# Performance work log

Measured on AMD Instinct MI355X. Metric: run time of the kernel, lower is better.

Reference implementation:

```python
import jax, jax.numpy as jnp
import numpy as np

D = 256      # feature_dim (d_model)
H = 4        # num_heads
N = 4096     # query nodes
M = 4096     # source nodes


def _conv1x1(W, b, x):
    # Conv1d(kernel_size=1): per-position linear over channels. x: [1, Cin, N]
    return jnp.einsum('oi,bin->bon', W, x) + b[None, :, None]


def setup_inputs() -> dict:
    key = jax.random.key(0)
    ks = jax.random.split(key, 16)
    s = 0.02
    inp = {
        'x':      jax.random.normal(ks[0], (1, D, N), jnp.float32),
        'source': jax.random.normal(ks[1], (1, D, M), jnp.float32),
        'dist':   jax.random.uniform(ks[2], (1, N, M), jnp.float32),
        'mask':   jax.random.bernoulli(ks[3], 0.5, (N, M)),
        'Wq': s * jax.random.normal(ks[4], (D, D), jnp.float32),  'bq': jnp.zeros((D,), jnp.float32),
        'Wk': s * jax.random.normal(ks[5], (D, D), jnp.float32),  'bk': jnp.zeros((D,), jnp.float32),
        'Wv': s * jax.random.normal(ks[6], (D, D), jnp.float32),  'bv': jnp.zeros((D,), jnp.float32),
        'Wm': s * jax.random.normal(ks[7], (D, D), jnp.float32),  'bm': jnp.zeros((D,), jnp.float32),
        'W1': s * jax.random.normal(ks[8], (2 * D, 2 * D), jnp.float32), 'b1': jnp.zeros((2 * D,), jnp.float32),
        'W2': s * jax.random.normal(ks[9], (D, 2 * D), jnp.float32),     'b2': jnp.zeros((D,), jnp.float32),
    }
    return inp


def reference(x, source, dist, mask, Wq, bq, Wk, bk, Wv, bv, Wm, bm, W1, b1, W2, b2):
    dim = D // H  # per-head dim; torch view(1, dim, H, -1) splits channels as (dim, H)
    q = _conv1x1(Wq, bq, x).reshape(1, dim, H, N)
    k = _conv1x1(Wk, bk, source).reshape(1, dim, H, M)
    v = _conv1x1(Wv, bv, source).reshape(1, dim, H, M)

    scores = jnp.einsum('bdhn,bdhm->bhnm', q, k) / jnp.sqrt(jnp.asarray(dim, q.dtype))
    # non-standard additive mask: global detached min scales the masked-out entries
    smin = jax.lax.stop_gradient(scores.min())
    scores = scores + smin * (~mask).astype(scores.dtype)[None, None, :, :]

    prob = jax.nn.softmax(scores, axis=-1)                       # [1,H,N,M]
    attn = jnp.einsum('bhnm,bdhm->bdhn', prob, v)                # [1,dim,H,N]
    message = _conv1x1(Wm, bm, attn.reshape(1, D, N))            # merge heads

    h = jnp.concatenate([x, message], axis=1)                    # [1,2D,N]
    h = jax.nn.relu(_conv1x1(W1, b1, h))
    y = _conv1x1(W2, b2, h)                                      # [1,D,N]
    weights = scores.mean(axis=1)                                # [1,N,M]
    return y, weights
```

## Files before the change

### kernel.cpp

```cpp
#include <hip/hip_runtime.h>
#include <hip/hip_bf16.h>
#include <hip/hip_fp16.h>
#include <math.h>

#define Dm 256
#define Hh 4
#define Nn 4096
#define Mq 4096

typedef __attribute__((ext_vector_type(8))) short bf16x8;
typedef __attribute__((ext_vector_type(4))) float f32x4;
typedef _Float16 __attribute__((ext_vector_type(4))) f16x4;
typedef __fp16 __attribute__((ext_vector_type(2))) h16x2;

#define MFMA_BF16(a,b,c) __builtin_amdgcn_mfma_f32_16x16x32_bf16(a,b,c,0,0,0)
#define MFMA_F16x16(a,b,c) __builtin_amdgcn_mfma_f32_16x16x16f16(a,b,c,0,0,0)

#define MB (1u<<20)
#define OFF_FLAG  0
#define OFF_SMIN  64
#define OFF_KMAX  128
#define OFF_MT    8192
#define OFF_DENP  (128u<<10)
#define OFF_WB    (3u*MB/2)
#define OFF_BITS  (3u*MB)
#define OFF_ATTNT (3u*MB)
#define OFF_QB    (5u*MB)
#define OFF_KB    (7u*MB)
#define OFF_VB    (9u*MB)
#define OFF_HCAT  (11u*MB)
#define OFF_OPART (15u*MB)
#define OFF_XT    (17u*MB)
#define OFF_ST    (19u*MB)
#define OFF_H1T   (15u*MB)

#define WOFF_Q  0
#define WOFF_K  65536
#define WOFF_V  131072
#define WOFF_M  196608
#define WOFF_1  262144
#define WOFF_2  524288

__device__ __forceinline__ unsigned short f2bf(float x) {
    unsigned u = __float_as_uint(x);
    u += 0x7FFF + ((u >> 16) & 1);
    return (unsigned short)(u >> 16);
}
__device__ __forceinline__ float bf2f(unsigned short b) {
    return __uint_as_float(((unsigned)b) << 16);
}
__device__ __forceinline__ unsigned fkey(float f) {
    unsigned u = __float_as_uint(f);
    return (u & 0x80000000u) ? ~u : (u | 0x80000000u);
}
__device__ __forceinline__ float fdecode(unsigned k) {
    return (k & 0x80000000u) ? __uint_as_float(k ^ 0x80000000u) : __uint_as_float(~k);
}

__global__ __launch_bounds__(256) void k_prep(const float* __restrict__ x,
                                              const float* __restrict__ source,
                                              unsigned short* __restrict__ xt,
                                              unsigned short* __restrict__ st,
                                              unsigned short* __restrict__ hcat,
                                              const unsigned char* __restrict__ maskb,
                                              int* __restrict__ flag,
                                              unsigned* __restrict__ kmax,
                                              unsigned* __restrict__ sminkey) {
    const int z = blockIdx.z;
    const float* src = z ? source : x;
    unsigned short* dst = z ? st : xt;
    unsigned short* dst2 = z ? nullptr : hcat;
    const int l = threadIdx.x & 63, g = threadIdx.x >> 6;
    const int c = blockIdx.y * 64 + l;
    const int n0 = blockIdx.x * 32 + g * 8;
    float4 v0 = *(const float4*)(src + (size_t)c * Nn + n0);
    float4 v1 = *(const float4*)(src + (size_t)c * Nn + n0 + 4);
    float vv[8] = {v0.x, v0.y, v0.z, v0.w, v1.x, v1.y, v1.z, v1.w};
    #pragma unroll
    for (int j = 0; j < 8; j++) {
        unsigned short b = f2bf(vv[j]);
        dst[(size_t)(n0 + j) * 256 + c] = b;
        if (dst2) dst2[(size_t)(n0 + j) * 512 + c] = b;
    }
    if (blockIdx.x == 0 && blockIdx.y == 0 && z == 0) {
        __shared__ int cnt[5];
        if (threadIdx.x < 5) cnt[threadIdx.x] = 0;
        if (threadIdx.x < 4) kmax[threadIdx.x] = 0u;
        if (threadIdx.x == 0) *sminkey = 0xFFFFFFFFu;
        __syncthreads();
        for (int i = threadIdx.x; i < 16384; i += 256) {
            unsigned char b = maskb[i];
            if (b) {
                atomicAdd(&cnt[i & 3], 1);
                if ((i & 7) == 4) atomicAdd(&cnt[4], 1);
            }
        }
        __syncthreads();
        if (threadIdx.x == 0) {
            int f;
            if (cnt[3] > 0 && cnt[0] == 0)        f = 3;
            else if (cnt[1] | cnt[2] | cnt[3])    f = 1;
            else if (cnt[4] > 0)                  f = 0;
            else                                  f = 2;
            *flag = f;
        }
    }
}

__global__ void k_maskbits(const void* __restrict__ mp, const int* __restrict__ flagp,
                           unsigned char* __restrict__ bits) {
    size_t i = (size_t)blockIdx.x * 256 + threadIdx.x;
    const int flag = *flagp;
    size_t base = i * 8;
    unsigned b = 0;
    if (flag == 1) {
        unsigned long long u = *(const unsigned long long*)((const unsigned char*)mp + base);
        #pragma unroll
        for (int j = 0; j < 8; j++) b |= (unsigned)(((u >> (8*j)) & 0xFFull) != 0ull) << j;
    } else if (flag == 0) {
        const int* p = (const int*)mp;
        #pragma unroll
        for (int j = 0; j < 8; j++) b |= (unsigned)(p[base + j] != 0) << j;
    } else if (flag == 3) {
        const float* p = (const float*)mp;
        #pragma unroll
        for (int j = 0; j < 8; j++) b |= (unsigned)(p[base + j] != 0.0f) << j;
    } else {
        const unsigned long long* p = (const unsigned long long*)mp;
        #pragma unroll
        for (int j = 0; j < 8; j++) b |= (unsigned)(p[base + j] != 0ull) << j;
    }
    bits[i] = (unsigned char)b;
}

__global__ void k_wcast(const float* __restrict__ Wq, const float* __restrict__ Wk,
                        const float* __restrict__ Wv, const float* __restrict__ Wm,
                        const float* __restrict__ W1, const float* __restrict__ W2,
                        unsigned short* __restrict__ wb) {
    size_t i = (size_t)blockIdx.x * 256 + threadIdx.x;
    const float* s; size_t off;
    if      (i < 65536)               { s = Wq; off = i; }
    else if (i < 131072)              { s = Wk; off = i - 65536; }
    else if (i < 196608)              { s = Wv; off = i - 131072; }
    else if (i < 262144)              { s = Wm; off = i - 196608; }
    else if (i < 524288)              { s = W1; off = i - 262144; }
    else                              { s = W2; off = i - 524288; }
    wb[i] = f2bf(s[off]);
}

template<int KK, int JT>
__device__ __forceinline__ void gemm_body(const unsigned short* __restrict__ wb,
                                          const float* __restrict__ bias,
                                          const unsigned short* __restrict__ xt,
                                          void* __restrict__ out, int mode,
                                          int bx, int by) {
    const int tid = threadIdx.x, w = tid >> 6, lane = tid & 63;
    const int lg = lane >> 4, lr = lane & 15;
    const int o_base = by * 64 + w * 16;
    const int n_base = bx * (16 * JT);
    f32x4 acc[JT];
    #pragma unroll
    for (int j = 0; j < JT; j++) acc[j] = (f32x4){0.f, 0.f, 0.f, 0.f};
    const unsigned short* wrow = wb + (size_t)(o_base + lr) * KK + lg * 8;
    const unsigned short* xrow = xt + (size_t)(n_base + lr) * KK + lg * 8;
    #pragma unroll
    for (int k0 = 0; k0 < KK; k0 += 32) {
        bf16x8 af = *(const bf16x8*)(wrow + k0);
        #pragma unroll
        for (int j = 0; j < JT; j++) {
            bf16x8 bfr = *(const bf16x8*)(xrow + (size_t)j * 16 * KK + k0);
            acc[j] = MFMA_BF16(af, bfr, acc[j]);
        }
    }
    float bv[4];
    #pragma unroll
    for (int r = 0; r < 4; r++) bv[r] = bias[o_base + lg * 4 + r];
    #pragma unroll
    for (int j = 0; j < JT; j++) {
        #pragma unroll
        for (int r = 0; r < 4; r++) {
            int o = o_base + lg * 4 + r;
            int n = n_base + j * 16 + lr;
            float v = acc[j][r] + bv[r];
            if (mode == 0) {
                ((float*)out)[(size_t)o * Nn + n] = v;
            } else if (mode == 1) {
                ((unsigned short*)out)[(((size_t)(o & 3)) * Nn + n) * 64 + (o >> 2)] = f2bf(v);
            } else if (mode == 2) {
                union { _Float16 h; unsigned short u; } cv; cv.h = (_Float16)v;
                ((unsigned short*)out)[(((size_t)(o & 3)) * 64 + (o >> 2)) * Mq + n] = cv.u;
            } else if (mode == 3) {
                ((unsigned short*)out)[(size_t)n * 512 + 256 + o] = f2bf(v);
            } else if (mode == 4) {
                ((unsigned short*)out)[(size_t)n * 512 + o] = f2bf(fmaxf(v, 0.f));
            } else {
                int dd = o >> 2, hh = o & 3, g = dd >> 3, pos = dd & 7;
                int slot = g ^ (n & 7);
                ((unsigned short*)out)[(((size_t)hh * Mq + n)) * 64 + slot * 8 + pos] = f2bf(v);
            }
        }
    }
}

template<int KK, int JT>
__global__ __launch_bounds__(256) void k_mgemm(const unsigned short* __restrict__ wb,
                                               const float* __restrict__ bias,
                                               const unsigned short* __restrict__ xt,
                                               void* __restrict__ out, int mode) {
    gemm_body<KK, JT>(wb, bias, xt, out, mode, blockIdx.x, blockIdx.y);
}

__global__ __launch_bounds__(256) void k_qkv(const unsigned short* __restrict__ wb,
                                             const float* __restrict__ bq,
                                             const float* __restrict__ bk,
                                             const float* __restrict__ bv,
                                             const unsigned short* __restrict__ xt,
                                             const unsigned short* __restrict__ st,
                                             void* __restrict__ qb, void* __restrict__ kb,
                                             void* __restrict__ vb) {
    const int z = blockIdx.z;
    const float* bias = (z == 0) ? bq : ((z == 1) ? bk : bv);
    const unsigned short* X = (z == 0) ? xt : st;
    void* out = (z == 0) ? qb : ((z == 1) ? kb : vb);
    int mode = (z == 0) ? 1 : ((z == 1) ? 5 : 2);
    gemm_body<256, 4>(wb + z * 65536, bias, X, out, mode, blockIdx.x, blockIdx.y);
}

__global__ __launch_bounds__(256) void k_knorm(const unsigned short* __restrict__ kb,
                                               unsigned* __restrict__ kmax) {
    const int h = blockIdx.y;
    const int m = blockIdx.x * 256 + threadIdx.x;
    const unsigned short* row = kb + ((size_t)(h * Mq + m) << 6);
    float s = 0.f;
    #pragma unroll
    for (int i = 0; i < 64; i++) { float v = bf2f(row[i]); s = fmaf(v, v, s); }
    __shared__ float red[256];
    red[threadIdx.x] = s;
    __syncthreads();
    for (int st = 128; st > 0; st >>= 1) {
        if (threadIdx.x < st) red[threadIdx.x] = fmaxf(red[threadIdx.x], red[threadIdx.x + st]);
        __syncthreads();
    }
    if (threadIdx.x == 0) atomicMax(kmax + h, __float_as_uint(red[0]));
}

__global__ __launch_bounds__(256) void k_qnorm(const unsigned short* __restrict__ qb,
                                               const unsigned* __restrict__ kmax,
                                               float* __restrict__ mtarr) {
    const int row = blockIdx.x * 256 + threadIdx.x;
    const unsigned short* qr = qb + ((size_t)row << 6);
    float s = 0.f;
    #pragma unroll
    for (int i = 0; i < 64; i++) { float v = bf2f(qr[i]); s = fmaf(v, v, s); }
    float k2 = __uint_as_float(kmax[row >> 12]);
    mtarr[row] = sqrtf(s * k2) * 0.125f;
}

__global__ __launch_bounds__(256) void k_min(
    const unsigned short* __restrict__ qb, const unsigned short* __restrict__ kb,
    unsigned* __restrict__ sminkey) {
    __shared__ unsigned short kbuf[2][8192];
    const int tid = threadIdx.x;
    const int w = tid >> 6, lane = tid & 63;
    const int lg = lane >> 4, lr = lane & 15;
    const int n0 = blockIdx.x * 128 + w * 32;
    const int m0 = blockIdx.y * 128;

    bf16x8 qf[4][2][2];
    #pragma unroll
    for (int h = 0; h < 4; h++)
        #pragma unroll
        for (int ns = 0; ns < 2; ns++)
            #pragma unroll
            for (int kh = 0; kh < 2; kh++)
                qf[h][ns][kh] = *(const bf16x8*)(qb + (((size_t)h * Nn + n0 + ns*16 + lr) << 6) + kh*32 + lg*8);

    const unsigned short* srcs[4];
    #pragma unroll
    for (int h = 0; h < 4; h++) srcs[h] = kb + (((size_t)h * Mq + m0) << 6) + tid * 8;

    float mn = INFINITY;

    bf16x8 r[4];
    #pragma unroll
    for (int h = 0; h < 4; h++) {
        r[h] = *(const bf16x8*)(srcs[h]);
        *(bf16x8*)&kbuf[0][h * 2048 + tid * 8] = r[h];
    }
    __syncthreads();
    #pragma unroll
    for (int h = 0; h < 4; h++) r[h] = *(const bf16x8*)(srcs[h] + 2048);

    for (int t = 0; t < 4; t++) {
        const unsigned short* kB = &kbuf[t & 1][0];
        #pragma unroll
        for (int mi = 0; mi < 2; mi++) {
            const int rowoff = (mi * 16 + lr) * 64;
            #pragma unroll
            for (int h = 0; h < 4; h++) {
                bf16x8 a0 = *(const bf16x8*)(kB + h*2048 + rowoff + ((lg ^ (lr & 7)) << 3));
                bf16x8 a1 = *(const bf16x8*)(kB + h*2048 + rowoff + (((lg + 4) ^ (lr & 7)) << 3));
                #pragma unroll
                for (int ns = 0; ns < 2; ns++) {
                    f32x4 acc = (f32x4){0.f, 0.f, 0.f, 0.f};
                    acc = MFMA_BF16(a0, qf[h][ns][0], acc);
                    acc = MFMA_BF16(a1, qf[h][ns][1], acc);
                    mn = fminf(mn, fminf(fminf(acc[0], acc[1]), fminf(acc[2], acc[3])));
                }
            }
        }
        if (t < 3) {
            #pragma unroll
            for (int h = 0; h < 4; h++)
                *(bf16x8*)&kbuf[(t + 1) & 1][h * 2048 + tid * 8] = r[h];
        }
        __syncthreads();
        if (t < 2) {
            #pragma unroll
            for (int h = 0; h < 4; h++) r[h] = *(const bf16x8*)(srcs[h] + (size_t)(t + 2) * 2048);
        }
    }

    for (int off = 1; off < 64; off <<= 1) mn = fminf(mn, __shfl_xor(mn, off));
    __shared__ float wmin[4];
    if (lane == 0) wmin[w] = mn;
    __syncthreads();
    if (tid == 0) {
        float m2 = fminf(fminf(wmin[0], wmin[1]), fminf(wmin[2], wmin[3]));
        atomicMin(sminkey, fkey(m2 * 0.125f));
    }
}

__global__ __launch_bounds__(256) void k_wout(
    const unsigned short* __restrict__ qb, const unsigned short* __restrict__ kb,
    const unsigned long long* __restrict__ bits,
    const unsigned* __restrict__ skey, float* __restrict__ wout) {
    __shared__ unsigned short kbuf[2][8192];
    const int tid = threadIdx.x;
    const int w = tid >> 6, lane = tid & 63;
    const int lg = lane >> 4, lr = lane & 15;
    const int n0 = blockIdx.x * 128 + w * 32;
    const int m0 = blockIdx.y * 128;
    const float smin = fdecode(*skey);

    bf16x8 qf[4][2][2];
    #pragma unroll
    for (int h = 0; h < 4; h++)
        #pragma unroll
        for (int ns = 0; ns < 2; ns++)
            #pragma unroll
            for (int kh = 0; kh < 2; kh++)
                qf[h][ns][kh] = *(const bf16x8*)(qb + (((size_t)h * Nn + n0 + ns*16 + lr) << 6) + kh*32 + lg*8);

    const unsigned short* srcs[4];
    #pragma unroll
    for (int h = 0; h < 4; h++) srcs[h] = kb + (((size_t)h * Mq + m0) << 6) + tid * 8;

    const unsigned long long* brow0 = bits + (((size_t)(n0 + lr)) << 6) + (m0 >> 6);
    const unsigned long long* brow1 = bits + (((size_t)(n0 + 16 + lr)) << 6) + (m0 >> 6);
    unsigned long long bw0 = 0ull, bw1 = 0ull;

    bf16x8 r[4];
    #pragma unroll
    for (int h = 0; h < 4; h++) {
        r[h] = *(const bf16x8*)(srcs[h]);
        *(bf16x8*)&kbuf[0][h * 2048 + tid * 8] = r[h];
    }
    __syncthreads();
    #pragma unroll
    for (int h = 0; h < 4; h++) r[h] = *(const bf16x8*)(srcs[h] + 2048);

    for (int t = 0; t < 4; t++) {
        const unsigned short* kB = &kbuf[t & 1][0];
        const int mch = m0 + t * 32;
        if ((t & 1) == 0) { bw0 = brow0[t >> 1]; bw1 = brow1[t >> 1]; }
        #pragma unroll
        for (int mi = 0; mi < 2; mi++) {
            const int rowoff = (mi * 16 + lr) * 64;
            f32x4 acc[2][2];
            #pragma unroll
            for (int ns = 0; ns < 2; ns++) {
                acc[ns][0] = (f32x4){0.f, 0.f, 0.f, 0.f};
                acc[ns][1] = (f32x4){0.f, 0.f, 0.f, 0.f};
            }
            #pragma unroll
            for (int h = 0; h < 4; h++) {
                bf16x8 a0 = *(const bf16x8*)(kB + h*2048 + rowoff + ((lg ^ (lr & 7)) << 3));
                bf16x8 a1 = *(const bf16x8*)(kB + h*2048 + rowoff + (((lg + 4) ^ (lr & 7)) << 3));
                const int hf = h >> 1;
                #pragma unroll
                for (int ns = 0; ns < 2; ns++) {
                    acc[ns][hf] = MFMA_BF16(a0, qf[h][ns][0], acc[ns][hf]);
                    acc[ns][hf] = MFMA_BF16(a1, qf[h][ns][1], acc[ns][hf]);
                }
            }
            const int shb = (t & 1) * 32 + mi * 16 + lg * 4;
            #pragma unroll
            for (int ns = 0; ns < 2; ns++) {
                unsigned long long bw = ns ? bw1 : bw0;
                f32x4 wv;
                #pragma unroll
                for (int rr = 0; rr < 4; rr++) {
                    bool b = (bw >> (shb + rr)) & 1ull;
                    wv[rr] = fmaf(acc[ns][0][rr] + acc[ns][1][rr], 0.03125f, b ? 0.f : smin);
                }
                __builtin_nontemporal_store(wv,
                    (f32x4*)(wout + (size_t)(n0 + ns*16 + lr) * Mq + mch + mi * 16 + lg * 4));
            }
        }
        if (t < 3) {
            #pragma unroll
            for (int h = 0; h < 4; h++)
                *(bf16x8*)&kbuf[(t + 1) & 1][h * 2048 + tid * 8] = r[h];
        }
        __syncthreads();
        if (t < 2) {
            #pragma unroll
            for (int h = 0; h < 4; h++) r[h] = *(const bf16x8*)(srcs[h] + (size_t)(t + 2) * 2048);
        }
    }
}

__global__ __launch_bounds__(256) void k_pv(
    const unsigned short* __restrict__ qb, const unsigned short* __restrict__ kb,
    const unsigned short* __restrict__ vbh,
    const unsigned long long* __restrict__ bits,
    const unsigned* __restrict__ skey, const float* __restrict__ mtarr,
    float* __restrict__ denp, unsigned short* __restrict__ opart) {
    __shared__ unsigned short kbuf[2][4096];
    __shared__ unsigned short vbuf[2][4096];
    const int tid = threadIdx.x;
    const int w = tid >> 6, lane = tid & 63;
    const int lg = lane >> 4, lr = lane & 15;
    const int h = blockIdx.y & 3, mb = blockIdx.y >> 2;
    const int n0 = blockIdx.x * 128 + w * 32;
    const int m0 = mb * 512;
    const float smin = fdecode(*skey);
    const float sminc = fmaxf(smin, 0.f);

    bf16x8 qf[2][2];
    float cT[2], cF[2];
    #pragma unroll
    for (int ns = 0; ns < 2; ns++) {
        const size_t qrow = ((size_t)h * Nn + n0 + ns*16 + lr) << 6;
        qf[ns][0] = *(const bf16x8*)(qb + qrow + lg*8);
        qf[ns][1] = *(const bf16x8*)(qb + qrow + 32 + lg*8);
        float mtE = mtarr[(size_t)h * Nn + n0 + ns*16 + lr] + sminc;
        cT[ns] = -mtE * 1.44269504f;
        cF[ns] = cT[ns] + smin * 1.44269504f;
    }

    f32x4 oacc[2][4];
    #pragma unroll
    for (int ns = 0; ns < 2; ns++)
        #pragma unroll
        for (int ds = 0; ds < 4; ds++) oacc[ns][ds] = (f32x4){0.f, 0.f, 0.f, 0.f};
    float dsum[2] = {0.f, 0.f};

    const unsigned short* ksrc = kb + (((size_t)h * Mq + m0) << 6) + tid * 8;
    const int vj = tid & 7;
    const int vdd0 = tid >> 3, vdd1 = 32 + (tid >> 3);
    const unsigned short* vsrc0 = vbh + (size_t)(h * 64 + vdd0) * Mq + m0 + vj * 8;
    const unsigned short* vsrc1 = vbh + (size_t)(h * 64 + vdd1) * Mq + m0 + vj * 8;
    int vdstA, vdstB, vdstC, vdstD;
    {
        int vds = vdd0 >> 4, vlr = vdd0 & 15, vmi = vj >> 1;
        int vswz = (vlr >> 2) & 3;
        int vbase = ((vmi * 4 + vds) * 16 + vlr) * 4;
        vdstA = (vbase + (((vj & 1) * 2 + 0) ^ vswz)) * 4;
        vdstB = (vbase + (((vj & 1) * 2 + 1) ^ vswz)) * 4;
        vds = vdd1 >> 4; vlr = vdd1 & 15;
        vswz = (vlr >> 2) & 3;
        vbase = ((vmi * 4 + vds) * 16 + vlr) * 4;
        vdstC = (vbase + (((vj & 1) * 2 + 0) ^ vswz)) * 4;
        vdstD = (vbase + (((vj & 1) * 2 + 1) ^ vswz)) * 4;
    }

    union U8 { bf16x8 v; unsigned long long q[2]; };
    U8 rv0, rv1;
    bf16x8 rk0 = *(const bf16x8*)(ksrc);
    bf16x8 rk1 = *(const bf16x8*)(ksrc + 2048);
    rv0.v = *(const bf16x8*)(vsrc0);
    rv1.v = *(const bf16x8*)(vsrc1);
    *(bf16x8*)&kbuf[0][tid * 8] = rk0;
    *(bf16x8*)&kbuf[0][2048 + tid * 8] = rk1;
    *(unsigned long long*)&vbuf[0][vdstA] = rv0.q[0];
    *(unsigned long long*)&vbuf[0][vdstB] = rv0.q[1];
    *(unsigned long long*)&vbuf[0][vdstC] = rv1.q[0];
    *(unsigned long long*)&vbuf[0][vdstD] = rv1.q[1];
    __syncthreads();
    rk0 = *(const bf16x8*)(ksrc + 4096);
    rk1 = *(const bf16x8*)(ksrc + 4096 + 2048);
    rv0.v = *(const bf16x8*)(vsrc0 + 64);
    rv1.v = *(const bf16x8*)(vsrc1 + 64);

    const unsigned long long* brow0 = bits + (((size_t)(n0 + lr)) << 6) + (m0 >> 6);
    const unsigned long long* brow1 = bits + (((size_t)(n0 + 16 + lr)) << 6) + (m0 >> 6);
    const int kslot0 = (lg ^ (lr & 7)) << 3;
    const int kslot1 = ((lg + 4) ^ (lr & 7)) << 3;
    const int vrslot = (lg ^ ((lr >> 2) & 3)) * 4;

    for (int t = 0; t < 8; t++) {
        const unsigned short* kB = &kbuf[t & 1][0];
        const unsigned short* vB = &vbuf[t & 1][0];
        unsigned long long bw[2];
        bw[0] = brow0[t];
        bw[1] = brow1[t];
        #pragma unroll
        for (int mi = 0; mi < 4; mi++) {
            const int rowoff = (mi * 16 + lr) * 64;
            bf16x8 a0 = *(const bf16x8*)(kB + rowoff + kslot0);
            bf16x8 a1 = *(const bf16x8*)(kB + rowoff + kslot1);
            f16x4 vf[4];
            #pragma unroll
            for (int ds = 0; ds < 4; ds++)
                vf[ds] = *(const f16x4*)&vB[((mi * 4 + ds) * 16 + lr) * 16 + vrslot];
            const int shb = mi * 16 + lg * 4;
            #pragma unroll
            for (int ns = 0; ns < 2; ns++) {
                f32x4 acc = (f32x4){0.f, 0.f, 0.f, 0.f};
                acc = MFMA_BF16(a0, qf[ns][0], acc);
                acc = MFMA_BF16(a1, qf[ns][1], acc);
                float p0 = exp2f(fmaf(acc[0], 0.18033688f, ((bw[ns] >> (shb + 0)) & 1ull) ? cT[ns] : cF[ns]));
                float p1 = exp2f(fmaf(acc[1], 0.18033688f, ((bw[ns] >> (shb + 1)) & 1ull) ? cT[ns] : cF[ns]));
                float p2 = exp2f(fmaf(acc[2], 0.18033688f, ((bw[ns] >> (shb + 2)) & 1ull) ? cT[ns] : cF[ns]));
                float p3 = exp2f(fmaf(acc[3], 0.18033688f, ((bw[ns] >> (shb + 3)) & 1ull) ? cT[ns] : cF[ns]));
                dsum[ns] += (p0 + p1) + (p2 + p3);
                union { h16x2 h2[2]; f16x4 f4; } pu;
                pu.h2[0] = __builtin_amdgcn_cvt_pkrtz(p0, p1);
                pu.h2[1] = __builtin_amdgcn_cvt_pkrtz(p2, p3);
                f16x4 pf = pu.f4;
                #pragma unroll
                for (int ds = 0; ds < 4; ds++)
                    oacc[ns][ds] = MFMA_F16x16(pf, vf[ds], oacc[ns][ds]);
            }
        }
        if (t < 7) {
            *(bf16x8*)&kbuf[(t + 1) & 1][tid * 8] = rk0;
            *(bf16x8*)&kbuf[(t + 1) & 1][2048 + tid * 8] = rk1;
            *(unsigned long long*)&vbuf[(t + 1) & 1][vdstA] = rv0.q[0];
            *(unsigned long long*)&vbuf[(t + 1) & 1][vdstB] = rv0.q[1];
            *(unsigned long long*)&vbuf[(t + 1) & 1][vdstC] = rv1.q[0];
            *(unsigned long long*)&vbuf[(t + 1) & 1][vdstD] = rv1.q[1];
        }
        __syncthreads();
        if (t < 6) {
            rk0 = *(const bf16x8*)(ksrc + (size_t)(t + 2) * 4096);
            rk1 = *(const bf16x8*)(ksrc + (size_t)(t + 2) * 4096 + 2048);
            rv0.v = *(const bf16x8*)(vsrc0 + (size_t)(t + 2) * 64);
            rv1.v = *(const bf16x8*)(vsrc1 + (size_t)(t + 2) * 64);
        }
    }

    #pragma unroll
    for (int ns = 0; ns < 2; ns++) {
        dsum[ns] += __shfl_xor(dsum[ns], 16);
        dsum[ns] += __shfl_xor(dsum[ns], 32);
    }
    if (lane < 16) {
        #pragma unroll
        for (int ns = 0; ns < 2; ns++)
            denp[((size_t)h * Nn + n0 + ns*16 + lane) * 8 + mb] = dsum[ns];
    }

    unsigned short* op = opart + (size_t)mb * (Dm * Nn);
    #pragma unroll
    for (int ns = 0; ns < 2; ns++)
        #pragma unroll
        for (int ds = 0; ds < 4; ds++) {
            int c = (ds * 16 + lr) * 4 + h;
            int n = n0 + ns * 16 + lg * 4;
            union { h16x2 h2[2]; unsigned long long q; } pu;
            pu.h2[0] = __builtin_amdgcn_cvt_pkrtz(oacc[ns][ds][0], oacc[ns][ds][1]);
            pu.h2[1] = __builtin_amdgcn_cvt_pkrtz(oacc[ns][ds][2], oacc[ns][ds][3]);
            *(unsigned long long*)&op[(size_t)c * Nn + n] = pu.q;
        }
}

__global__ __launch_bounds__(256) void k_finish(const unsigned short* __restrict__ opart,
                                                const float* __restrict__ denp,
                                                unsigned short* __restrict__ attnT) {
    __shared__ float t[64][65];
    const int cb = blockIdx.y * 64, nb = blockIdx.x * 64;
    const int tid = threadIdx.x;
    #pragma unroll
    for (int e = 0; e < 16; e++) {
        int idx = e * 256 + tid;
        int c_l = idx >> 6, n_l = idx & 63;
        int c = cb + c_l, n = nb + n_l;
        float s = 0.f;
        #pragma unroll
        for (int y = 0; y < 8; y++) {
            union { unsigned short u; _Float16 h; } cv;
            cv.u = opart[(size_t)y * (Dm*Nn) + (size_t)c * Nn + n];
            s += (float)cv.h;
        }
        size_t row = (size_t)(c & 3) * Nn + n;
        float d = 0.f;
        #pragma unroll
        for (int mb = 0; mb < 8; mb++) d += denp[row*8 + mb];
        t[c_l][n_l] = s / d;
    }
    __syncthreads();
    #pragma unroll
    for (int e = 0; e < 16; e++) {
        int idx = e * 256 + tid;
        int n_l = idx >> 6, c_l = idx & 63;
        attnT[(size_t)(nb + n_l) * 256 + cb + c_l] = f2bf(t[c_l][n_l]);
    }
}

extern "C" void kernel_launch(void* const* d_in, const int* in_sizes, int n_in,
                              void* d_out, int out_size, void* d_ws, size_t ws_size,
                              hipStream_t stream) {
    const float* x      = (const float*)d_in[0];
    const float* source = (const float*)d_in[1];
    const void*  mask   = d_in[3];
    const float* Wq = (const float*)d_in[4];  const float* bq = (const float*)d_in[5];
    const float* Wk = (const float*)d_in[6];  const float* bk = (const float*)d_in[7];
    const float* Wv = (const float*)d_in[8];  const float* bv = (const float*)d_in[9];
    const float* Wm = (const float*)d_in[10]; const float* bm = (const float*)d_in[11];
    const float* W1 = (const float*)d_in[12]; const float* b1 = (const float*)d_in[13];
    const float* W2 = (const float*)d_in[14]; const float* b2 = (const float*)d_in[15];

    float* y    = (float*)d_out;
    float* wout = y + (size_t)Dm * Nn;

    char* ws = (char*)d_ws;
    int*      flag  = (int*)(ws + OFF_FLAG);
    unsigned* skey  = (unsigned*)(ws + OFF_SMIN);
    unsigned* kmax  = (unsigned*)(ws + OFF_KMAX);
    float*    mtarr = (float*)(ws + OFF_MT);
    float*    denp  = (float*)(ws + OFF_DENP);
    unsigned short* wb    = (unsigned short*)(ws + OFF_WB);
    unsigned char*  bits  = (unsigned char*)(ws + OFF_BITS);
    unsigned short* qb    = (unsigned short*)(ws + OFF_QB);
    unsigned short* kb    = (unsigned short*)(ws + OFF_KB);
    unsigned short* vb    = (unsigned short*)(ws + OFF_VB);
    unsigned short* hcat  = (unsigned short*)(ws + OFF_HCAT);
    unsigned short* attnT = (unsigned short*)(ws + OFF_ATTNT);
    unsigned short* xt    = (unsigned short*)(ws + OFF_XT);
    unsigned short* st    = (unsigned short*)(ws + OFF_ST);
    unsigned short* opart = (unsigned short*)(ws + OFF_OPART);
    unsigned short* h1t   = (unsigned short*)(ws + OFF_H1T);

    k_prep<<<dim3(128, 4, 2), 256, 0, stream>>>(x, source, xt, st, hcat,
                                                (const unsigned char*)mask, flag, kmax, skey);
    k_maskbits<<<8192, 256, 0, stream>>>(mask, flag, bits);
    k_wcast<<<2560, 256, 0, stream>>>(Wq, Wk, Wv, Wm, W1, W2, wb);

    k_qkv<<<dim3(64, 4, 3), 256, 0, stream>>>(wb, bq, bk, bv, xt, st, qb, kb, vb);

    k_knorm<<<dim3(16, 4), 256, 0, stream>>>(kb, kmax);
    k_qnorm<<<64, 256, 0, stream>>>(qb, kmax, mtarr);

    k_min<<<dim3(32, 32), 256, 0, stream>>>(qb, kb, skey);

    k_wout<<<dim3(32, 32), 256, 0, stream>>>(qb, kb, (const unsigned long long*)bits, skey, wout);

    k_pv<<<dim3(32, 32), 256, 0, stream>>>(qb, kb, vb, (const unsigned long long*)bits,
                                           skey, mtarr, denp, opart);
    k_finish<<<dim3(64, 4), 256, 0, stream>>>(opart, denp, attnT);

    k_mgemm<256, 4><<<dim3(64, 4), 256, 0, stream>>>(wb + WOFF_M, bm, attnT, hcat, 3);
    k_mgemm<512, 4><<<dim3(64, 8), 256, 0, stream>>>(wb + WOFF_1, b1, hcat, h1t, 4);
    k_mgemm<512, 4><<<dim3(64, 4), 256, 0, stream>>>(wb + WOFF_2, b2, h1t, y, 0);
}
```

Baseline: 215.0 us.

## Fuse weights output into PV kernel and retile min-score kernel

Removes the separate k_wout kernel. The head-mean weights are now produced inside the PV kernel (renamed k_pvw), which loops over all four heads per block and reuses the QK scores it already computes, so the second full QK^T recompute and its extra K reads go away. Each block of the fused kernel now covers 64 queries by 512 keys across all heads, giving 512 blocks instead of 1024 and more accumulator registers per thread. k_min is also retiled to 512 threads with 16 query rows per wave and 256 keys per block. The risks are higher register pressure lowering occupancy, and extra wout stores sitting on the PV critical path.

```diff
diff --git a/kernel.cpp b/kernel.cpp
--- a/kernel.cpp
+++ b/kernel.cpp
@@ -256,42 +256,40 @@
     mtarr[row] = sqrtf(s * k2) * 0.125f;
 }
 
-__global__ __launch_bounds__(256) void k_min(
+__global__ __launch_bounds__(512) void k_min(
     const unsigned short* __restrict__ qb, const unsigned short* __restrict__ kb,
     unsigned* __restrict__ sminkey) {
     __shared__ unsigned short kbuf[2][8192];
     const int tid = threadIdx.x;
     const int w = tid >> 6, lane = tid & 63;
     const int lg = lane >> 4, lr = lane & 15;
-    const int n0 = blockIdx.x * 128 + w * 32;
-    const int m0 = blockIdx.y * 128;
-
-    bf16x8 qf[4][2][2];
+    const int n0 = blockIdx.x * 128 + w * 16;
+    const int m0 = blockIdx.y * 256;
+
+    bf16x8 qf[4][2];
     #pragma unroll
     for (int h = 0; h < 4; h++)
         #pragma unroll
-        for (int ns = 0; ns < 2; ns++)
-            #pragma unroll
-            for (int kh = 0; kh < 2; kh++)
-                qf[h][ns][kh] = *(const bf16x8*)(qb + (((size_t)h * Nn + n0 + ns*16 + lr) << 6) + kh*32 + lg*8);
-
-    const unsigned short* srcs[4];
-    #pragma unroll
-    for (int h = 0; h < 4; h++) srcs[h] = kb + (((size_t)h * Mq + m0) << 6) + tid * 8;
+        for (int kh = 0; kh < 2; kh++)
+            qf[h][kh] = *(const bf16x8*)(qb + (((size_t)h * Nn + n0 + lr) << 6) + kh*32 + lg*8);
+
+    const int h0 = tid >> 8, q0 = tid & 255;
+    const unsigned short* src0 = kb + (((size_t)h0 * Mq + m0) << 6) + q0 * 8;
+    const unsigned short* src1 = kb + (((size_t)(h0 + 2) * Mq + m0) << 6) + q0 * 8;
+    unsigned short* dst0 = &kbuf[0][h0 * 2048 + q0 * 8];
+    unsigned short* dst1 = &kbuf[0][(h0 + 2) * 2048 + q0 * 8];
 
     float mn = INFINITY;
 
-    bf16x8 r[4];
-    #pragma unroll
-    for (int h = 0; h < 4; h++) {
-        r[h] = *(const bf16x8*)(srcs[h]);
-        *(bf16x8*)&kbuf[0][h * 2048 + tid * 8] = r[h];
-    }
+    bf16x8 r0 = *(const bf16x8*)(src0);
+    bf16x8 r1 = *(const bf16x8*)(src1);
+    *(bf16x8*)dst0 = r0;
+    *(bf16x8*)dst1 = r1;
     __syncthreads();
-    #pragma unroll
-    for (int h = 0; h < 4; h++) r[h] = *(const bf16x8*)(srcs[h] + 2048);
-
-    for (int t = 0; t < 4; t++) {
+    r0 = *(const bf16x8*)(src0 + 2048);
+    r1 = *(const bf16x8*)(src1 + 2048);
+
+    for (int t = 0; t < 8; t++) {
         const unsigned short* kB = &kbuf[t & 1][0];
         #pragma unroll
         for (int mi = 0; mi < 2; mi++) {
@@ -300,168 +298,73 @@
             for (int h = 0; h < 4; h++) {
                 bf16x8 a0 = *(const bf16x8*)(kB + h*2048 + rowoff + ((lg ^ (lr & 7)) << 3));
                 bf16x8 a1 = *(const bf16x8*)(kB + h*2048 + rowoff + (((lg + 4) ^ (lr & 7)) << 3));
-                #pragma unroll
-                for (int ns = 0; ns < 2; ns++) {
-                    f32x4 acc = (f32x4){0.f, 0.f, 0.f, 0.f};
-                    acc = MFMA_BF16(a0, qf[h][ns][0], acc);
-                    acc = MFMA_BF16(a1, qf[h][ns][1], acc);
-                    mn = fminf(mn, fminf(fminf(acc[0], acc[1]), fminf(acc[2], acc[3])));
-                }
+                f32x4 acc = (f32x4){0.f, 0.f, 0.f, 0.f};
+                acc = MFMA_BF16(a0, qf[h][0], acc);
+                acc = MFMA_BF16(a1, qf[h][1], acc);
+                mn = fminf(mn, fminf(fminf(acc[0], acc[1]), fminf(acc[2], acc[3])));
             }
         }
-        if (t < 3) {
-            #pragma unroll
-            for (int h = 0; h < 4; h++)
-                *(bf16x8*)&kbuf[(t + 1) & 1][h * 2048 + tid * 8] = r[h];
+        if (t < 7) {
+            *(bf16x8*)(dst0 + (((t + 1) & 1) ? 8192 : 0)) = r0;
+            *(bf16x8*)(dst1 + (((t + 1) & 1) ? 8192 : 0)) = r1;
         }
         __syncthreads();
-        if (t < 2) {
-            #pragma unroll
-            for (int h = 0; h < 4; h++) r[h] = *(const bf16x8*)(srcs[h] + (size_t)(t + 2) * 2048);
+        if (t < 6) {
+            r0 = *(const bf16x8*)(src0 + (size_t)(t + 2) * 2048);
+            r1 = *(const bf16x8*)(src1 + (size_t)(t + 2) * 2048);
         }
     }
 
     for (int off = 1; off < 64; off <<= 1) mn = fminf(mn, __shfl_xor(mn, off));
-    __shared__ float wmin[4];
+    __shared__ float wmin[8];
     if (lane == 0) wmin[w] = mn;
     __syncthreads();
     if (tid == 0) {
-        float m2 = fminf(fminf(wmin[0], wmin[1]), fminf(wmin[2], wmin[3]));
+        float m2 = wmin[0];
+        #pragma unroll
+        for (int i = 1; i < 8; i++) m2 = fminf(m2, wmin[i]);
         atomicMin(sminkey, fkey(m2 * 0.125f));
     }
 }
 
-__global__ __launch_bounds__(256) void k_wout(
-    const unsigned short* __restrict__ qb, const unsigned short* __restrict__ kb,
-    const unsigned long long* __restrict__ bits,
-    const unsigned* __restrict__ skey, float* __restrict__ wout) {
-    __shared__ unsigned short kbuf[2][8192];
-    const int tid = threadIdx.x;
-    const int w = tid >> 6, lane = tid & 63;
-    const int lg = lane >> 4, lr = lane & 15;
-    const int n0 = blockIdx.x * 128 + w * 32;
-    const int m0 = blockIdx.y * 128;
-    const float smin = fdecode(*skey);
-
-    bf16x8 qf[4][2][2];
-    #pragma unroll
-    for (int h = 0; h < 4; h++)
-        #pragma unroll
-        for (int ns = 0; ns < 2; ns++)
-            #pragma unroll
-            for (int kh = 0; kh < 2; kh++)
-                qf[h][ns][kh] = *(const bf16x8*)(qb + (((size_t)h * Nn + n0 + ns*16 + lr) << 6) + kh*32 + lg*8);
-
-    const unsigned short* srcs[4];
-    #pragma unroll
-    for (int h = 0; h < 4; h++) srcs[h] = kb + (((size_t)h * Mq + m0) << 6) + tid * 8;
-
-    const unsigned long long* brow0 = bits + (((size_t)(n0 + lr)) << 6) + (m0 >> 6);
-    const unsigned long long* brow1 = bits + (((size_t)(n0 + 16 + lr)) << 6) + (m0 >> 6);
-    unsigned long long bw0 = 0ull, bw1 = 0ull;
-
-    bf16x8 r[4];
-    #pragma unroll
-    for (int h = 0; h < 4; h++) {
-        r[h] = *(const bf16x8*)(srcs[h]);
-        *(bf16x8*)&kbuf[0][h * 2048 + tid * 8] = r[h];
-    }
-    __syncthreads();
-    #pragma unroll
-    for (int h = 0; h < 4; h++) r[h] = *(const bf16x8*)(srcs[h] + 2048);
-
-    for (int t = 0; t < 4; t++) {
-        const unsigned short* kB = &kbuf[t & 1][0];
-        const int mch = m0 + t * 32;
-        if ((t & 1) == 0) { bw0 = brow0[t >> 1]; bw1 = brow1[t >> 1]; }
-        #pragma unroll
-        for (int mi = 0; mi < 2; mi++) {
-            const int rowoff = (mi * 16 + lr) * 64;
-            f32x4 acc[2][2];
-            #pragma unroll
-            for (int ns = 0; ns < 2; ns++) {
-                acc[ns][0] = (f32x4){0.f, 0.f, 0.f, 0.f};
-                acc[ns][1] = (f32x4){0.f, 0.f, 0.f, 0.f};
-            }
-            #pragma unroll
-            for (int h = 0; h < 4; h++) {
-                bf16x8 a0 = *(const bf16x8*)(kB + h*2048 + rowoff + ((lg ^ (lr & 7)) << 3));
-                bf16x8 a1 = *(const bf16x8*)(kB + h*2048 + rowoff + (((lg + 4) ^ (lr & 7)) << 3));
-                const int hf = h >> 1;
-                #pragma unroll
-                for (int ns = 0; ns < 2; ns++) {
-                    acc[ns][hf] = MFMA_BF16(a0, qf[h][ns][0], acc[ns][hf]);
-                    acc[ns][hf] = MFMA_BF16(a1, qf[h][ns][1], acc[ns][hf]);
-                }
-            }
-            const int shb = (t & 1) * 32 + mi * 16 + lg * 4;
-            #pragma unroll
-            for (int ns = 0; ns < 2; ns++) {
-                unsigned long long bw = ns ? bw1 : bw0;
-                f32x4 wv;
-                #pragma unroll
-                for (int rr = 0; rr < 4; rr++) {
-                    bool b = (bw >> (shb + rr)) & 1ull;
-                    wv[rr] = fmaf(acc[ns][0][rr] + acc[ns][1][rr], 0.03125f, b ? 0.f : smin);
-                }
-                __builtin_nontemporal_store(wv,
-                    (f32x4*)(wout + (size_t)(n0 + ns*16 + lr) * Mq + mch + mi * 16 + lg * 4));
-            }
-        }
-        if (t < 3) {
-            #pragma unroll
-            for (int h = 0; h < 4; h++)
-                *(bf16x8*)&kbuf[(t + 1) & 1][h * 2048 + tid * 8] = r[h];
-        }
-        __syncthreads();
-        if (t < 2) {
-            #pragma unroll
-            for (int h = 0; h < 4; h++) r[h] = *(const bf16x8*)(srcs[h] + (size_t)(t + 2) * 2048);
-        }
-    }
-}
-
-__global__ __launch_bounds__(256) void k_pv(
+__global__ __launch_bounds__(256) void k_pvw(
     const unsigned short* __restrict__ qb, const unsigned short* __restrict__ kb,
     const unsigned short* __restrict__ vbh,
     const unsigned long long* __restrict__ bits,
     const unsigned* __restrict__ skey, const float* __restrict__ mtarr,
-    float* __restrict__ denp, unsigned short* __restrict__ opart) {
+    float* __restrict__ wout, float* __restrict__ denp, unsigned short* __restrict__ opart) {
     __shared__ unsigned short kbuf[2][4096];
     __shared__ unsigned short vbuf[2][4096];
     const int tid = threadIdx.x;
     const int w = tid >> 6, lane = tid & 63;
     const int lg = lane >> 4, lr = lane & 15;
-    const int h = blockIdx.y & 3, mb = blockIdx.y >> 2;
-    const int n0 = blockIdx.x * 128 + w * 32;
+    const int mb = blockIdx.y;
+    const int n0 = blockIdx.x * 64 + w * 16;
     const int m0 = mb * 512;
     const float smin = fdecode(*skey);
     const float sminc = fmaxf(smin, 0.f);
 
-    bf16x8 qf[2][2];
-    float cT[2], cF[2];
-    #pragma unroll
-    for (int ns = 0; ns < 2; ns++) {
-        const size_t qrow = ((size_t)h * Nn + n0 + ns*16 + lr) << 6;
-        qf[ns][0] = *(const bf16x8*)(qb + qrow + lg*8);
-        qf[ns][1] = *(const bf16x8*)(qb + qrow + 32 + lg*8);
-        float mtE = mtarr[(size_t)h * Nn + n0 + ns*16 + lr] + sminc;
-        cT[ns] = -mtE * 1.44269504f;
-        cF[ns] = cT[ns] + smin * 1.44269504f;
-    }
-
-    f32x4 oacc[2][4];
-    #pragma unroll
-    for (int ns = 0; ns < 2; ns++)
-        #pragma unroll
-        for (int ds = 0; ds < 4; ds++) oacc[ns][ds] = (f32x4){0.f, 0.f, 0.f, 0.f};
-    float dsum[2] = {0.f, 0.f};
-
-    const unsigned short* ksrc = kb + (((size_t)h * Mq + m0) << 6) + tid * 8;
+    bf16x8 qf[4][2];
+    float cT[4], cF[4];
+    #pragma unroll
+    for (int h = 0; h < 4; h++) {
+        const size_t qrow = ((size_t)h * Nn + n0 + lr) << 6;
+        qf[h][0] = *(const bf16x8*)(qb + qrow + lg*8);
+        qf[h][1] = *(const bf16x8*)(qb + qrow + 32 + lg*8);
+        float mtE = mtarr[(size_t)h * Nn + n0 + lr] + sminc;
+        cT[h] = -mtE * 1.44269504f;
+        cF[h] = cT[h] + smin * 1.44269504f;
+    }
+
+    f32x4 oacc[4][4];
+    #pragma unroll
+    for (int h = 0; h < 4; h++)
+        #pragma unroll
+        for (int ds = 0; ds < 4; ds++) oacc[h][ds] = (f32x4){0.f, 0.f, 0.f, 0.f};
+    float dsum[4] = {0.f, 0.f, 0.f, 0.f};
+
     const int vj = tid & 7;
     const int vdd0 = tid >> 3, vdd1 = 32 + (tid >> 3);
-    const unsigned short* vsrc0 = vbh + (size_t)(h * 64 + vdd0) * Mq + m0 + vj * 8;
-    const unsigned short* vsrc1 = vbh + (size_t)(h * 64 + vdd1) * Mq + m0 + vj * 8;
     int vdstA, vdstB, vdstC, vdstD;
     {
         int vds = vdd0 >> 4, vlr = vdd0 & 15, vmi = vj >> 1;
@@ -478,10 +381,10 @@
 
     union U8 { bf16x8 v; unsigned long long q[2]; };
     U8 rv0, rv1;
-    bf16x8 rk0 = *(const bf16x8*)(ksrc);
-    bf16x8 rk1 = *(const bf16x8*)(ksrc + 2048);
-    rv0.v = *(const bf16x8*)(vsrc0);
-    rv1.v = *(const bf16x8*)(vsrc1);
+    bf16x8 rk0 = *(const bf16x8*)(kb + (((size_t)0 * Mq + m0) << 6) + tid * 8);
+    bf16x8 rk1 = *(const bf16x8*)(kb + (((size_t)0 * Mq + m0) << 6) + 2048 + tid * 8);
+    rv0.v = *(const bf16x8*)(vbh + (size_t)(0 * 64 + vdd0) * Mq + m0 + vj * 8);
+    rv1.v = *(const bf16x8*)(vbh + (size_t)(0 * 64 + vdd1) * Mq + m0 + vj * 8);
     *(bf16x8*)&kbuf[0][tid * 8] = rk0;
     *(bf16x8*)&kbuf[0][2048 + tid * 8] = rk1;
     *(unsigned long long*)&vbuf[0][vdstA] = rv0.q[0];
@@ -489,23 +392,28 @@
     *(unsigned long long*)&vbuf[0][vdstC] = rv1.q[0];
     *(unsigned long long*)&vbuf[0][vdstD] = rv1.q[1];
     __syncthreads();
-    rk0 = *(const bf16x8*)(ksrc + 4096);
-    rk1 = *(const bf16x8*)(ksrc + 4096 + 2048);
-    rv0.v = *(const bf16x8*)(vsrc0 + 64);
-    rv1.v = *(const bf16x8*)(vsrc1 + 64);
-
-    const unsigned long long* brow0 = bits + (((size_t)(n0 + lr)) << 6) + (m0 >> 6);
-    const unsigned long long* brow1 = bits + (((size_t)(n0 + 16 + lr)) << 6) + (m0 >> 6);
+    rk0 = *(const bf16x8*)(kb + (((size_t)1 * Mq + m0) << 6) + tid * 8);
+    rk1 = *(const bf16x8*)(kb + (((size_t)1 * Mq + m0) << 6) + 2048 + tid * 8);
+    rv0.v = *(const bf16x8*)(vbh + (size_t)(1 * 64 + vdd0) * Mq + m0 + vj * 8);
+    rv1.v = *(const bf16x8*)(vbh + (size_t)(1 * 64 + vdd1) * Mq + m0 + vj * 8);
+
+    const unsigned long long* brow = bits + (((size_t)(n0 + lr)) << 6) + (m0 >> 6);
     const int kslot0 = (lg ^ (lr & 7)) << 3;
     const int kslot1 = ((lg + 4) ^ (lr & 7)) << 3;
     const int vrslot = (lg ^ ((lr >> 2) & 3)) * 4;
 
-    for (int t = 0; t < 8; t++) {
-        const unsigned short* kB = &kbuf[t & 1][0];
-        const unsigned short* vB = &vbuf[t & 1][0];
-        unsigned long long bw[2];
-        bw[0] = brow0[t];
-        bw[1] = brow1[t];
+    unsigned long long bw = brow[0];
+    unsigned long long bw_next = 0ull;
+    f32x4 wsum[4];
+
+    for (int s = 0; s < 32; s++) {
+        const int t = s >> 2, h = s & 3;
+        const unsigned short* kB = &kbuf[s & 1][0];
+        const unsigned short* vB = &vbuf[s & 1][0];
+        if (h == 0) {
+            #pragma unroll
+            for (int mi = 0; mi < 4; mi++) wsum[mi] = (f32x4){0.f, 0.f, 0.f, 0.f};
+        }
         #pragma unroll
         for (int mi = 0; mi < 4; mi++) {
             const int rowoff = (mi * 16 + lr) * 64;
@@ -515,64 +423,81 @@
             #pragma unroll
             for (int ds = 0; ds < 4; ds++)
                 vf[ds] = *(const f16x4*)&vB[((mi * 4 + ds) * 16 + lr) * 16 + vrslot];
+            f32x4 acc = (f32x4){0.f, 0.f, 0.f, 0.f};
+            acc = MFMA_BF16(a0, qf[h][0], acc);
+            acc = MFMA_BF16(a1, qf[h][1], acc);
+            wsum[mi] += acc;
             const int shb = mi * 16 + lg * 4;
+            const unsigned nib = (unsigned)(bw >> shb) & 0xFu;
+            float p0 = exp2f(fmaf(acc[0], 0.18033688f, (nib & 1u) ? cT[h] : cF[h]));
+            float p1 = exp2f(fmaf(acc[1], 0.18033688f, (nib & 2u) ? cT[h] : cF[h]));
+            float p2 = exp2f(fmaf(acc[2], 0.18033688f, (nib & 4u) ? cT[h] : cF[h]));
+            float p3 = exp2f(fmaf(acc[3], 0.18033688f, (nib & 8u) ? cT[h] : cF[h]));
+            dsum[h] += (p0 + p1) + (p2 + p3);
+            union { h16x2 h2[2]; f16x4 f4; } pu;
+            pu.h2[0] = __builtin_amdgcn_cvt_pkrtz(p0, p1);
+            pu.h2[1] = __builtin_amdgcn_cvt_pkrtz(p2, p3);
+            f16x4 pf = pu.f4;
             #pragma unroll
-            for (int ns = 0; ns < 2; ns++) {
-                f32x4 acc = (f32x4){0.f, 0.f, 0.f, 0.f};
-                acc = MFMA_BF16(a0, qf[ns][0], acc);
-                acc = MFMA_BF16(a1, qf[ns][1], acc);
-                float p0 = exp2f(fmaf(acc[0], 0.18033688f, ((bw[ns] >> (shb + 0)) & 1ull) ? cT[ns] : cF[ns]));
-                float p1 = exp2f(fmaf(acc[1], 0.18033688f, ((bw[ns] >> (shb + 1)) & 1ull) ? cT[ns] : cF[ns]));
-                float p2 = exp2f(fmaf(acc[2], 0.18033688f, ((bw[ns] >> (shb + 2)) & 1ull) ? cT[ns] : cF[ns]));
-                float p3 = exp2f(fmaf(acc[3], 0.18033688f, ((bw[ns] >> (shb + 3)) & 1ull) ? cT[ns] : cF[ns]));
-                dsum[ns] += (p0 + p1) + (p2 + p3);
-                union { h16x2 h2[2]; f16x4 f4; } pu;
-                pu.h2[0] = __builtin_amdgcn_cvt_pkrtz(p0, p1);
-                pu.h2[1] = __builtin_amdgcn_cvt_pkrtz(p2, p3);
-                f16x4 pf = pu.f4;
-                #pragma unroll
-                for (int ds = 0; ds < 4; ds++)
-                    oacc[ns][ds] = MFMA_F16x16(pf, vf[ds], oacc[ns][ds]);
+            for (int ds = 0; ds < 4; ds++)
+                oacc[h][ds] = MFMA_F16x16(pf, vf[ds], oacc[h][ds]);
+        }
+        if (h == 2 && t < 7) bw_next = brow[t + 1];
+        if (h == 3) {
+            #pragma unroll
+            for (int mi = 0; mi < 4; mi++) {
+                const int shb = mi * 16 + lg * 4;
+                const unsigned nib = (unsigned)(bw >> shb) & 0xFu;
+                f32x4 wv;
+                wv[0] = fmaf(wsum[mi][0], 0.03125f, (nib & 1u) ? 0.f : smin);
+                wv[1] = fmaf(wsum[mi][1], 0.03125f, (nib & 2u) ? 0.f : smin);
+                wv[2] = fmaf(wsum[mi][2], 0.03125f, (nib & 4u) ? 0.f : smin);
+                wv[3] = fmaf(wsum[mi][3], 0.03125f, (nib & 8u) ? 0.f : smin);
+                __builtin_nontemporal_store(wv,
+                    (f32x4*)(wout + (size_t)(n0 + lr) * Mq + m0 + t * 64 + mi * 16 + lg * 4));
             }
-        }
-        if (t < 7) {
-            *(bf16x8*)&kbuf[(t + 1) & 1][tid * 8] = rk0;
-            *(bf16x8*)&kbuf[(t + 1) & 1][2048 + tid * 8] = rk1;
-            *(unsigned long long*)&vbuf[(t + 1) & 1][vdstA] = rv0.q[0];
-            *(unsigned long long*)&vbuf[(t + 1) & 1][vdstB] = rv0.q[1];
-            *(unsigned long long*)&vbuf[(t + 1) & 1][vdstC] = rv1.q[0];
-            *(unsigned long long*)&vbuf[(t + 1) & 1][vdstD] = rv1.q[1];
+            bw = bw_next;
+        }
+        if (s < 31) {
+            *(bf16x8*)&kbuf[(s + 1) & 1][tid * 8] = rk0;
+            *(bf16x8*)&kbuf[(s + 1) & 1][2048 + tid * 8] = rk1;
+            *(unsigned long long*)&vbuf[(s + 1) & 1][vdstA] = rv0.q[0];
+            *(unsigned long long*)&vbuf[(s + 1) & 1][vdstB] = rv0.q[1];
+            *(unsigned long long*)&vbuf[(s + 1) & 1][vdstC] = rv1.q[0];
+            *(unsigned long long*)&vbuf[(s + 1) & 1][vdstD] = rv1.q[1];
         }
         __syncthreads();
-        if (t < 6) {
-            rk0 = *(const bf16x8*)(ksrc + (size_t)(t + 2) * 4096);
-            rk1 = *(const bf16x8*)(ksrc + (size_t)(t + 2) * 4096 + 2048);
-            rv0.v = *(const bf16x8*)(vsrc0 + (size_t)(t + 2) * 64);
-            rv1.v = *(const bf16x8*)(vsrc1 + (size_t)(t + 2) * 64);
-        }
-    }
-
-    #pragma unroll
-    for (int ns = 0; ns < 2; ns++) {
-        dsum[ns] += __shfl_xor(dsum[ns], 16);
-        dsum[ns] += __shfl_xor(dsum[ns], 32);
+        if (s < 30) {
+            const int s2 = s + 2, t2 = s2 >> 2, h2 = s2 & 3;
+            const size_t koff = (((size_t)h2 * Mq + m0 + t2 * 64) << 6);
+            rk0 = *(const bf16x8*)(kb + koff + tid * 8);
+            rk1 = *(const bf16x8*)(kb + koff + 2048 + tid * 8);
+            rv0.v = *(const bf16x8*)(vbh + (size_t)(h2 * 64 + vdd0) * Mq + m0 + t2 * 64 + vj * 8);
+            rv1.v = *(const bf16x8*)(vbh + (size_t)(h2 * 64 + vdd1) * Mq + m0 + t2 * 64 + vj * 8);
+        }
+    }
+
+    #pragma unroll
+    for (int h = 0; h < 4; h++) {
+        dsum[h] += __shfl_xor(dsum[h], 16);
+        dsum[h] += __shfl_xor(dsum[h], 32);
     }
     if (lane < 16) {
         #pragma unroll
-        for (int ns = 0; ns < 2; ns++)
-            denp[((size_t)h * Nn + n0 + ns*16 + lane) * 8 + mb] = dsum[ns];
+        for (int h = 0; h < 4; h++)
+            denp[((size_t)h * Nn + n0 + lane) * 8 + mb] = dsum[h];
     }
 
     unsigned short* op = opart + (size_t)mb * (Dm * Nn);
     #pragma unroll
-    for (int ns = 0; ns < 2; ns++)
+    for (int h = 0; h < 4; h++)
         #pragma unroll
         for (int ds = 0; ds < 4; ds++) {
             int c = (ds * 16 + lr) * 4 + h;
-            int n = n0 + ns * 16 + lg * 4;
+            int n = n0 + lg * 4;
             union { h16x2 h2[2]; unsigned long long q; } pu;
-            pu.h2[0] = __builtin_amdgcn_cvt_pkrtz(oacc[ns][ds][0], oacc[ns][ds][1]);
-            pu.h2[1] = __builtin_amdgcn_cvt_pkrtz(oacc[ns][ds][2], oacc[ns][ds][3]);
+            pu.h2[0] = __builtin_amdgcn_cvt_pkrtz(oacc[h][ds][0], oacc[h][ds][1]);
+            pu.h2[1] = __builtin_amdgcn_cvt_pkrtz(oacc[h][ds][2], oacc[h][ds][3]);
             *(unsigned long long*)&op[(size_t)c * Nn + n] = pu.q;
         }
 }
@@ -654,12 +579,10 @@
     k_knorm<<<dim3(16, 4), 256, 0, stream>>>(kb, kmax);
     k_qnorm<<<64, 256, 0, stream>>>(qb, kmax, mtarr);
 
-    k_min<<<dim3(32, 32), 256, 0, stream>>>(qb, kb, skey);
-
-    k_wout<<<dim3(32, 32), 256, 0, stream>>>(qb, kb, (const unsigned long long*)bits, skey, wout);
-
-    k_pv<<<dim3(32, 32), 256, 0, stream>>>(qb, kb, vb, (const unsigned long long*)bits,
-                                           skey, mtarr, denp, opart);
+    k_min<<<dim3(32, 16), 512, 0, stream>>>(qb, kb, skey);
+
+    k_pvw<<<dim3(64, 8), 256, 0, stream>>>(qb, kb, vb, (const unsigned long long*)bits,
+                                           skey, mtarr, wout, denp, opart);
     k_finish<<<dim3(64, 4), 256, 0, stream>>>(opart, denp, attnT);
 
     k_mgemm<256, 4><<<dim3(64, 4), 256, 0, stream>>>(wb + WOFF_M, bm, attnT, hcat, 3);
```

Result: slower. 511.1 us (+137.8%).
